# Performance work log

Hardware: AMD Instinct MI355X
Metric: run time of the kernel (lower is better)

Reference implementation:

```python
import jax, jax.numpy as jnp
import numpy as np

B, T, N, IN_DIM, H, C, L, S, P = 64, 13, 325, 2, 64, 4, 2, 4, 12
NC = S * N  # combined temporal-graph node count per batch element


def _make_adj(rng, n, density=0.03):
    mask = rng.random((n, n)) < density
    return (mask * rng.random((n, n))).astype(np.float32)


def _combine(adj, s, forward):
    n = adj.shape[0]
    out = np.zeros((n * s, n * s), np.float32)
    for i in range(s):
        out[i * n:(i + 1) * n, i * n:(i + 1) * n] = adj
        if forward and i < s - 1:
            out[i * n:(i + 1) * n, (i + 1) * n:(i + 2) * n] = np.eye(n, dtype=np.float32)
    return out


def _checkpoints(s, t):
    mark, cp = s, []
    while mark < t:
        cp.append(mark)
        mark += s - 1
    if cp[-1] != t:
        cp.append(t)
    return cp


def setup_inputs():
    key = jax.random.key(0)
    ks = jax.random.split(key, 20)
    rng = np.random.default_rng(0)
    adj = _make_adj(rng, N)
    pea = _make_adj(rng, N)
    sc = 0.05
    inp = {
        'inputs': jax.random.normal(ks[0], (B, T, N, IN_DIM), jnp.float32),
        'adj_fwd': jnp.asarray(_combine(adj, S, True)),
        'adj_bwd': jnp.asarray(_combine(adj, S, False)),
        'pea_fwd': jnp.asarray(_combine(pea, S, True)),
        'pea_bwd': jnp.asarray(_combine(pea, S, False)),
        'w_in': sc * jax.random.normal(ks[1], (IN_DIM, H), jnp.float32),
        'b_in': jnp.zeros((H,), jnp.float32),
        'res_w': sc * jax.random.normal(ks[2], (S,), jnp.float32),
        'res_b': jnp.zeros((), jnp.float32),
        'gconv_w': sc * jax.random.normal(ks[3], (S,), jnp.float32),
        'gconv_b': jnp.zeros((), jnp.float32),
        'gate1_w': sc * jax.random.normal(ks[4], (H, H), jnp.float32),
        'gate1_b': jnp.zeros((H,), jnp.float32),
        'gate2_w': sc * jax.random.normal(ks[5], (H, H * C), jnp.float32),
        'gate2_b': jnp.zeros((H * C,), jnp.float32),
        'reduce_w': sc * jax.random.normal(ks[6], (C * H, H), jnp.float32),
        'reduce_b': jnp.zeros((H,), jnp.float32),
        'gcn_adj_w': sc * jax.random.normal(ks[7], (C, L, 2, H, H), jnp.float32),
        'gcn_adj_b': jnp.zeros((C, L, H), jnp.float32),
        'gcn_pea_w': sc * jax.random.normal(ks[8], (C, L, 2, H, H), jnp.float32),
        'gcn_pea_b': jnp.zeros((C, L, H), jnp.float32),
        'out_conv_w': sc * jax.random.normal(ks[9], (P,), jnp.float32),
        'out_conv_b': jnp.zeros((P,), jnp.float32),
        'out_lin_w': sc * jax.random.normal(ks[10], (H, 1), jnp.float32),
        'out_lin_b': jnp.zeros((1,), jnp.float32),
    }
    return inp


def _gcn_stack(feats, W, b, A_f, A_b, n_out):
    # feats [B, S*N, H]; W [L, 2, H, H]; weighted message passing over both supports
    h = feats
    for l in range(W.shape[0]):
        mf = jnp.einsum('nm,bmh->bnh', A_f, h)
        mb = jnp.einsum('nm,bmh->bnh', A_b, h)
        h = jax.nn.relu(mf @ W[l, 0] + mb @ W[l, 1] + b[l])
    return h[:, -n_out:, :]  # last snapshot's nodes -> [B, N, H]


def reference(inputs, adj_fwd, adj_bwd, pea_fwd, pea_bwd, w_in, b_in, res_w, res_b,
              gconv_w, gconv_b, gate1_w, gate1_b, gate2_w, gate2_b, reduce_w, reduce_b,
              gcn_adj_w, gcn_adj_b, gcn_pea_w, gcn_pea_b, out_conv_w, out_conv_b,
              out_lin_w, out_lin_b):
    b_, t_, n_, _ = inputs.shape
    h_ = w_in.shape[1]
    s_ = res_w.shape[0]
    c_ = gcn_adj_w.shape[0]
    x = inputs @ w_in + b_in  # [B, T, N, H]
    last = None
    left = 0
    for idx, right in enumerate(_checkpoints(s_, t_)):
        fs = x[:, left:right] if idx == 0 else jnp.concatenate([last, x[:, left:right]], axis=1)  # [B,S,N,H]
        gf = (jnp.einsum('s,bsnh->bnh', gconv_w, fs) + gconv_b).reshape(b_ * n_, h_)
        residual = jnp.einsum('s,bsnh->bnh', res_w, fs) + res_b  # [B,N,H]
        feats = fs.reshape(b_, s_ * n_, h_)
        ca = jnp.concatenate(
            [_gcn_stack(feats, gcn_adj_w[c], gcn_adj_b[c], adj_fwd, adj_bwd, n_) for c in range(c_)],
            axis=-1).reshape(b_ * n_, c_ * h_)
        cp = jnp.concatenate(
            [_gcn_stack(feats, gcn_pea_w[c], gcn_pea_b[c], pea_fwd, pea_bwd, n_) for c in range(c_)],
            axis=-1).reshape(b_ * n_, c_ * h_)
        gate = jax.nn.sigmoid(jax.nn.relu(gf @ gate1_w + gate1_b) @ gate2_w + gate2_b)
        gr = gate * ca + (1.0 - gate) * cp
        gr = (gr @ reduce_w + reduce_b).reshape(b_, n_, h_)
        cr = gr + residual
        # nn.LayerNorm([B, N, H], elementwise_affine=False): normalize over whole tensor
        mu = jnp.mean(cr)
        var = jnp.var(cr)
        last = ((cr - mu) * jax.lax.rsqrt(var + 1e-5))[:, None]  # [B,1,N,H]
        left = right
    # 1x1 conv 1->pred_len over channel dim, then linear H->1
    out = jax.nn.relu(out_conv_w.reshape(1, -1, 1, 1) * last + out_conv_b.reshape(1, -1, 1, 1))
    out = out @ out_lin_w + out_lin_b  # [B, pred_len, N, 1]
    return out
```

## Files before the change

### kernel.cpp

```cpp
#include <hip/hip_runtime.h>
#include <hip/hip_bf16.h>
#include <math.h>

#define B_    64
#define T_    13
#define N_    325
#define H_    64
#define C_    4
#define L_    2
#define S_    4
#define P_    12
#define KCP   4
#define M_    (B_*N_)
#define ADJLD 1300
#define NNZCAP 64
#define WPITCH 72
#define MTP   264
#define RTP   264
#define NBLK  1300
#define MIXG  1304

typedef short bfrag __attribute__((ext_vector_type(8)));
typedef float f32x4 __attribute__((ext_vector_type(4)));

__device__ __forceinline__ void fma4(float4& a, float s, float4 x) {
    a.x += s * x.x; a.y += s * x.y; a.z += s * x.z; a.w += s * x.w;
}
__device__ __forceinline__ ushort bf_rne(float f) {
    unsigned u = __float_as_uint(f);
    return (ushort)((u + 0x7fffu + ((u >> 16) & 1u)) >> 16);
}
__device__ __forceinline__ uint2 pack_bf4(float4 v) {
    unsigned a = __float_as_uint(v.x), b = __float_as_uint(v.y);
    unsigned c = __float_as_uint(v.z), d = __float_as_uint(v.w);
    a = (a + 0x7fffu + ((a >> 16) & 1u)) >> 16;
    b = (b + 0x7fffu + ((b >> 16) & 1u)) >> 16;
    c = (c + 0x7fffu + ((c >> 16) & 1u)) >> 16;
    d = (d + 0x7fffu + ((d >> 16) & 1u)) >> 16;
    return make_uint2(a | (b << 16), c | (d << 16));
}
__device__ __forceinline__ float4 unpack_bf4(uint2 p) {
    return make_float4(__uint_as_float(p.x << 16),
                       __uint_as_float(p.x & 0xffff0000u),
                       __uint_as_float(p.y << 16),
                       __uint_as_float(p.y & 0xffff0000u));
}

__global__ void k_setup(
    const float* __restrict__ adj_fwd, const float* __restrict__ pea_fwd,
    const float* __restrict__ inp,
    const float* __restrict__ w_in, const float* __restrict__ b_in,
    const float* __restrict__ gadj_w, const float* __restrict__ gpea_w,
    const float* __restrict__ reduce_w,
    const float* __restrict__ gate1_w, const float* __restrict__ gate2_w,
    int* __restrict__ cnt, int* __restrict__ cols, float* __restrict__ vals,
    ushort* __restrict__ g_init4, ushort* __restrict__ WT,
    ushort* __restrict__ RT, ushort* __restrict__ W1T, ushort* __restrict__ W2T)
{
    int bid = blockIdx.x, t = threadIdx.x;
    if (bid >= 182) {
        int idx = (bid - 182) * 256 + t;
        if (idx >= 4 * M_ * H_) return;
        int h  = idx & 63;
        int r  = idx >> 6;
        int it = r / M_;
        int m  = r - it * M_;
        int b  = m / N_, n = m % N_;
        int tt = 3 * it + 3;
        const float* ip = inp + ((size_t)(b * T_ + tt) * N_ + n) * 2;
        g_init4[idx] = bf_rne(ip[0] * w_in[h] + ip[1] * w_in[H_ + h] + b_in[h]);
    } else if (bid < 163) {
        int lane = t & 63, w = t >> 6;
        int row = bid * 4 + w;
        if (row >= 2 * N_) return;
        int mat = (row >= N_) ? 1 : 0;
        int n   = row - mat * N_;
        const float* A = mat ? pea_fwd : adj_fwd;
        const float* rp = A + (size_t)n * ADJLD;
        int* cw   = cols + (size_t)row * NNZCAP;
        float* vw = vals + (size_t)row * NNZCAP;
        int c = 0;
        for (int c0 = 0; c0 < 384; c0 += 64) {
            int col = c0 + lane;
            float v = (col < N_) ? rp[col] : 0.f;
            unsigned long long mmask = __ballot(v != 0.f);
            int idx = c + __popcll(mmask & ((1ull << lane) - 1ull));
            if (v != 0.f && idx < NNZCAP) { cw[idx] = col; vw[idx] = v; }
            c += __popcll(mmask);
        }
        if (c + lane < NNZCAP) { cw[c + lane] = 0; vw[c + lane] = 0.f; }
        if (lane == 0) cnt[row] = (c < NNZCAP) ? c : NNZCAP;
    } else if (bid == 163) {
        for (int i = 0; i < 64; ++i) {
            int e = t + i * 256;
            int k = e >> 6, n = e & 63;
            RT[(size_t)n * RTP + k] = bf_rne(reduce_w[e]);
        }
    } else if (bid < 180) {
        int mat = bid - 164;
        int layer = mat >> 3, sm = mat & 7;
        int stack = sm >> 2, c = sm & 3;
        const float* w0 = (stack ? gpea_w : gadj_w) + (size_t)((c * L_ + layer) * 2) * 4096;
        const float* w1 = w0 + 4096;
        for (int i = 0; i < 16; ++i) {
            int e = t + i * 256;
            int k = e >> 6, n = e & 63;
            WT[((size_t)mat * 64 + n) * WPITCH + k] = bf_rne(w0[e] + w1[e]);
        }
    } else if (bid == 180) {
        for (int i = 0; i < 16; ++i) {
            int e = t + i * 256;
            int k = e >> 6, n = e & 63;
            W1T[(size_t)n * WPITCH + k] = bf_rne(gate1_w[e]);
        }
    } else {
        for (int i = 0; i < 64; ++i) {
            int e = t + i * 256;
            int k = e >> 8, n = e & 255;
            W2T[(size_t)n * WPITCH + k] = bf_rne(gate2_w[e]);
        }
    }
}

__device__ __forceinline__ void l1_block(
    int vb, int t,
    const int*   __restrict__ cnt,
    const int*   __restrict__ cols,
    const float* __restrict__ vals,
    const ushort* __restrict__ g_init,
    const ushort* __restrict__ WT,
    const float* __restrict__ badj, const float* __restrict__ bpea,
    ushort* __restrict__ G1a, ushort* __restrict__ G1p,
    ushort* MaH, ushort* MpH)
{
    int lane = t & 63, w = t >> 6;
    int m0 = vb * 32;
    int q = lane >> 4, ml = lane & 15;
    int colg = w * 16 + ml;

    bfrag BF[8][2];
    #pragma unroll
    for (int mat = 0; mat < 8; ++mat)
        #pragma unroll
        for (int kc = 0; kc < 2; ++kc)
            BF[mat][kc] = *(const bfrag*)&WT[((size_t)mat * 64 + colg) * WPITCH + kc * 32 + q * 8];

    {
        int cl = lane & 15, rr = lane >> 4;
        int mA = m0 + w * 8 + rr;
        int mB = mA + 4;
        int nA = mA % N_, nB = mB % N_;
        const ushort* gA = g_init + (size_t)(mA - nA) * H_ + cl * 4;
        const ushort* gB = g_init + (size_t)(mB - nB) * H_ + cl * 4;
        const int   *cA0 = cols + nA * NNZCAP,        *cB0 = cols + nB * NNZCAP;
        const float *vA0 = vals + nA * NNZCAP,        *vB0 = vals + nB * NNZCAP;
        const int   *cA1 = cols + (N_ + nA) * NNZCAP, *cB1 = cols + (N_ + nB) * NNZCAP;
        const float *vA1 = vals + (N_ + nA) * NNZCAP, *vB1 = vals + (N_ + nB) * NNZCAP;
        int jm = max(max(cnt[nA], cnt[nB]), max(cnt[N_ + nA], cnt[N_ + nB]));
        float4 aA0 = make_float4(0.f,0.f,0.f,0.f), aB0 = make_float4(0.f,0.f,0.f,0.f);
        float4 aA1 = make_float4(0.f,0.f,0.f,0.f), aB1 = make_float4(0.f,0.f,0.f,0.f);
        for (int j = 0; j < jm; j += 2) {
            fma4(aA0, vA0[j],   unpack_bf4(*(const uint2*)&gA[cA0[j]   * H_]));
            fma4(aA0, vA0[j+1], unpack_bf4(*(const uint2*)&gA[cA0[j+1] * H_]));
            fma4(aB0, vB0[j],   unpack_bf4(*(const uint2*)&gB[cB0[j]   * H_]));
            fma4(aB0, vB0[j+1], unpack_bf4(*(const uint2*)&gB[cB0[j+1] * H_]));
            fma4(aA1, vA1[j],   unpack_bf4(*(const uint2*)&gA[cA1[j]   * H_]));
            fma4(aA1, vA1[j+1], unpack_bf4(*(const uint2*)&gA[cA1[j+1] * H_]));
            fma4(aB1, vB1[j],   unpack_bf4(*(const uint2*)&gB[cB1[j]   * H_]));
            fma4(aB1, vB1[j+1], unpack_bf4(*(const uint2*)&gB[cB1[j+1] * H_]));
        }
        *(uint2*)&MaH[(w * 8 + rr) * WPITCH + cl * 4]     = pack_bf4(aA0);
        *(uint2*)&MaH[(w * 8 + 4 + rr) * WPITCH + cl * 4] = pack_bf4(aB0);
        *(uint2*)&MpH[(w * 8 + rr) * WPITCH + cl * 4]     = pack_bf4(aA1);
        *(uint2*)&MpH[(w * 8 + 4 + rr) * WPITCH + cl * 4] = pack_bf4(aB1);
    }
    __syncthreads();

    #pragma unroll
    for (int sc = 0; sc < 8; ++sc) {
        int stack = sc >> 2, c = sc & 3;
        const ushort* Msrc = stack ? MpH : MaH;
        float bv = (stack ? bpea : badj)[c * L_ * H_ + colg];
        ushort* Gout = stack ? G1p : G1a;
        #pragma unroll
        for (int r = 0; r < 2; ++r) {
            bfrag A0 = *(const bfrag*)&Msrc[(16 * r + ml) * WPITCH + q * 8];
            bfrag A1 = *(const bfrag*)&Msrc[(16 * r + ml) * WPITCH + 32 + q * 8];
            f32x4 acc = {0.f, 0.f, 0.f, 0.f};
            acc = __builtin_amdgcn_mfma_f32_16x16x32_bf16(A0, BF[sc][0], acc, 0, 0, 0);
            acc = __builtin_amdgcn_mfma_f32_16x16x32_bf16(A1, BF[sc][1], acc, 0, 0, 0);
            #pragma unroll
            for (int j = 0; j < 4; ++j) {
                float v = acc[j] + bv;
                v = v > 0.f ? v : 0.f;
                Gout[(size_t)(m0 + 16 * r + q * 4 + j) * 256 + c * 64 + colg] = bf_rne(v);
            }
        }
    }
}

__global__ __launch_bounds__(256, 4) void k_layer1(
    const int*   __restrict__ cnt,
    const int*   __restrict__ cols,
    const float* __restrict__ vals,
    const ushort* __restrict__ g_init4,
    int it0,
    const ushort* __restrict__ WT,
    const float* __restrict__ badj, const float* __restrict__ bpea,
    ushort* __restrict__ G1a4, ushort* __restrict__ G1p4)
{
    __shared__ __align__(16) ushort MaH[32 * WPITCH];
    __shared__ __align__(16) ushort MpH[32 * WPITCH];
    int itk = blockIdx.x / 656;
    int lx  = blockIdx.x - itk * 656;
    int vb = (lx & 7) * 82 + (lx >> 3);
    if (vb >= 650) return;
    l1_block(vb, threadIdx.x, cnt, cols, vals,
             g_init4 + (size_t)(it0 + itk) * M_ * H_, WT, badj, bpea,
             G1a4 + (size_t)itk * M_ * 256, G1p4 + (size_t)itk * M_ * 256,
             MaH, MpH);
}

__global__ __launch_bounds__(256, 4) void k_mix(
    const float* __restrict__ inp,
    const float* __restrict__ w_in, const float* __restrict__ b_in,
    const float* __restrict__ gconv_w, const float* __restrict__ gconv_b,
    const float* __restrict__ res_w,   const float* __restrict__ res_b,
    const float* __restrict__ cr_in, int it,
    const ushort* __restrict__ W1T, const float* __restrict__ b1,
    const ushort* __restrict__ W2T, const float* __restrict__ b2,
    const int*   __restrict__ cnt,
    const int*   __restrict__ cols,
    const float* __restrict__ vals,
    const ushort* __restrict__ G1a, const ushort* __restrict__ G1p,
    const ushort* __restrict__ WT,
    const float* __restrict__ badj, const float* __restrict__ bpea,
    const ushort* __restrict__ RT,
    const float* __restrict__ reduce_b,
    float* __restrict__ cr,
    const float* __restrict__ partials_in,
    float* __restrict__ partials,
    const ushort* __restrict__ g_init_l1,
    ushort* __restrict__ G1a_wr, ushort* __restrict__ G1p_wr)
{
    __shared__ __align__(16) ushort MtA[16 * MTP];
    __shared__ __align__(16) ushort MtP[16 * MTP];
    __shared__ __align__(16) ushort Gf[16 * WPITCH];
    __shared__ __align__(16) ushort Gr[16 * WPITCH];
    __shared__ float RES[16 * 68];
    __shared__ float red[8];
    int t = threadIdx.x, lane = t & 63, w = t >> 6;

    if (blockIdx.x >= MIXG) {
        int lx = blockIdx.x - MIXG;
        int vb1 = (lx & 7) * 82 + (lx >> 3);
        if (vb1 >= 650) return;
        l1_block(vb1, t, cnt, cols, vals, g_init_l1, WT, badj, bpea,
                 G1a_wr, G1p_wr, (ushort*)MtA, (ushort*)MtP);
        return;
    }

    int vb = (blockIdx.x & 7) * 163 + (blockIdx.x >> 3);
    if (vb >= NBLK) return;
    int m0 = vb * 16;
    int q = lane >> 4, ml = lane & 15;
    int colg = w * 16 + ml;

    float mu = 0.f, rs = 0.f;
    if (it > 0) {
        float a = 0.f, b = 0.f;
        for (int i = t; i < NBLK; i += 256) { a += partials_in[i]; b += partials_in[NBLK + i]; }
        #pragma unroll
        for (int off = 32; off > 0; off >>= 1) {
            a += __shfl_xor(a, off);
            b += __shfl_xor(b, off);
        }
        if (lane == 0) { red[w] = a; red[4 + w] = b; }
        __syncthreads();
        a = red[0] + red[1] + red[2] + red[3];
        b = red[4] + red[5] + red[6] + red[7];
        const float inv = 1.f / (float)(M_ * H_);
        mu = a * inv;
        float var = b * inv - mu * mu;
        rs = rsqrtf(var + 1e-5f);
    }

    {
        float wa = w_in[lane], wb = w_in[H_ + lane], bi = b_in[lane];
        float gw0 = gconv_w[0], gw1 = gconv_w[1], gw2 = gconv_w[2], gw3 = gconv_w[3];
        float rw0 = res_w[0],   rw1 = res_w[1],   rw2 = res_w[2],   rw3 = res_w[3];
        float gb = gconv_b[0],  rb = res_b[0];
        int t1 = (it == 0) ? 1 : (3 * it + 1);
        for (int i = 0; i < 4; ++i) {
            int r = i * 4 + w;
            int m = m0 + r;
            int b = m / N_, n = m % N_;
            const float* ipb = inp + ((size_t)b * T_ * N_ + n) * 2;
            float v0;
            if (it > 0) v0 = (cr_in[(size_t)m * H_ + lane] - mu) * rs;
            else        v0 = ipb[0] * wa + ipb[1] * wb + bi;
            const float* ip1 = ipb + (size_t)t1 * N_ * 2;
            const float* ip2 = ip1 + (size_t)N_ * 2;
            const float* ip3 = ip2 + (size_t)N_ * 2;
            float v1 = ip1[0] * wa + ip1[1] * wb + bi;
            float v2 = ip2[0] * wa + ip2[1] * wb + bi;
            float v3 = ip3[0] * wa + ip3[1] * wb + bi;
            Gf[r * WPITCH + lane] = bf_rne(gb + gw0 * v0 + gw1 * v1 + gw2 * v2 + gw3 * v3);
            RES[r * 68 + lane]    = rb + rw0 * v0 + rw1 * v1 + rw2 * v2 + rw3 * v3;
        }
    }
    __syncthreads();

    {
        bfrag A0 = *(const bfrag*)&Gf[ml * WPITCH + q * 8];
        bfrag A1 = *(const bfrag*)&Gf[ml * WPITCH + 32 + q * 8];
        bfrag B0 = *(const bfrag*)&W1T[(size_t)colg * WPITCH + q * 8];
        bfrag B1 = *(const bfrag*)&W1T[(size_t)colg * WPITCH + 32 + q * 8];
        f32x4 acc = {0.f, 0.f, 0.f, 0.f};
        acc = __builtin_amdgcn_mfma_f32_16x16x32_bf16(A0, B0, acc, 0, 0, 0);
        acc = __builtin_amdgcn_mfma_f32_16x16x32_bf16(A1, B1, acc, 0, 0, 0);
        float bb = b1[colg];
        #pragma unroll
        for (int j = 0; j < 4; ++j) {
            float v = acc[j] + bb;
            v = v > 0.f ? v : 0.f;
            Gr[(q * 4 + j) * WPITCH + colg] = bf_rne(v);
        }
    }
    __syncthreads();

    f32x4 gsv[4];
    {
        bfrag A0 = *(const bfrag*)&Gr[ml * WPITCH + q * 8];
        bfrag A1 = *(const bfrag*)&Gr[ml * WPITCH + 32 + q * 8];
        #pragma unroll
        for (int c = 0; c < 4; ++c) {
            bfrag B0 = *(const bfrag*)&W2T[(size_t)(c * 64 + colg) * WPITCH + q * 8];
            bfrag B1 = *(const bfrag*)&W2T[(size_t)(c * 64 + colg) * WPITCH + 32 + q * 8];
            f32x4 acc = {0.f, 0.f, 0.f, 0.f};
            acc = __builtin_amdgcn_mfma_f32_16x16x32_bf16(A0, B0, acc, 0, 0, 0);
            acc = __builtin_amdgcn_mfma_f32_16x16x32_bf16(A1, B1, acc, 0, 0, 0);
            float bb = b2[c * 64 + colg];
            #pragma unroll
            for (int j = 0; j < 4; ++j)
                gsv[c][j] = 1.f / (1.f + expf(-(acc[j] + bb)));
        }
    }

    for (int pp = 0; pp < 4; pp += 2) {
        int ma = m0 + w * 4 + pp, mb = ma + 1;
        int na = ma % N_, nb = mb % N_;
        const ushort* ga = G1a + (size_t)(ma - na) * 256 + lane * 4;
        const ushort* gb = G1a + (size_t)(mb - nb) * 256 + lane * 4;
        const ushort* pa = G1p + (size_t)(ma - na) * 256 + lane * 4;
        const ushort* pb = G1p + (size_t)(mb - nb) * 256 + lane * 4;
        const int   *cA0 = cols + na * NNZCAP,        *cB0 = cols + nb * NNZCAP;
        const float *vA0 = vals + na * NNZCAP,        *vB0 = vals + nb * NNZCAP;
        const int   *cA1 = cols + (N_ + na) * NNZCAP, *cB1 = cols + (N_ + nb) * NNZCAP;
        const float *vA1 = vals + (N_ + na) * NNZCAP, *vB1 = vals + (N_ + nb) * NNZCAP;
        int jm = max(max(cnt[na], cnt[nb]), max(cnt[N_ + na], cnt[N_ + nb]));
        float4 a0 = make_float4(0.f,0.f,0.f,0.f), a1 = make_float4(0.f,0.f,0.f,0.f);
        float4 p0 = make_float4(0.f,0.f,0.f,0.f), p1 = make_float4(0.f,0.f,0.f,0.f);
        for (int j = 0; j < jm; j += 2) {
            fma4(a0, vA0[j],   unpack_bf4(*(const uint2*)&ga[cA0[j]   * 256]));
            fma4(a0, vA0[j+1], unpack_bf4(*(const uint2*)&ga[cA0[j+1] * 256]));
            fma4(a1, vB0[j],   unpack_bf4(*(const uint2*)&gb[cB0[j]   * 256]));
            fma4(a1, vB0[j+1], unpack_bf4(*(const uint2*)&gb[cB0[j+1] * 256]));
            fma4(p0, vA1[j],   unpack_bf4(*(const uint2*)&pa[cA1[j]   * 256]));
            fma4(p0, vA1[j+1], unpack_bf4(*(const uint2*)&pa[cA1[j+1] * 256]));
            fma4(p1, vB1[j],   unpack_bf4(*(const uint2*)&pb[cB1[j]   * 256]));
            fma4(p1, vB1[j+1], unpack_bf4(*(const uint2*)&pb[cB1[j+1] * 256]));
        }
        int row0 = w * 4 + pp;
        *(uint2*)&MtA[row0 * MTP + lane * 4]       = pack_bf4(a0);
        *(uint2*)&MtA[(row0 + 1) * MTP + lane * 4] = pack_bf4(a1);
        *(uint2*)&MtP[row0 * MTP + lane * 4]       = pack_bf4(p0);
        *(uint2*)&MtP[(row0 + 1) * MTP + lane * 4] = pack_bf4(p1);
    }
    __syncthreads();

    const ushort* WT1 = WT + (size_t)8 * 64 * WPITCH;
    f32x4 res[4];
    bfrag B0c = *(const bfrag*)&WT1[(size_t)colg * WPITCH + q * 8];
    bfrag B1c = *(const bfrag*)&WT1[(size_t)colg * WPITCH + 32 + q * 8];
    #pragma unroll
    for (int sc = 0; sc < 8; ++sc) {
        int stack = sc >> 2, c = sc & 3;
        bfrag B0n = B0c, B1n = B1c;
        if (sc < 7) {
            B0n = *(const bfrag*)&WT1[((size_t)(sc + 1) * 64 + colg) * WPITCH + q * 8];
            B1n = *(const bfrag*)&WT1[((size_t)(sc + 1) * 64 + colg) * WPITCH + 32 + q * 8];
        }
        const ushort* Msrc = stack ? MtP : MtA;
        float bv = (stack ? bpea : badj)[(c * L_ + 1) * H_ + colg];
        bfrag A0 = *(const bfrag*)&Msrc[ml * MTP + c * 64 + q * 8];
        bfrag A1 = *(const bfrag*)&Msrc[ml * MTP + c * 64 + 32 + q * 8];
        f32x4 acc = {0.f, 0.f, 0.f, 0.f};
        acc = __builtin_amdgcn_mfma_f32_16x16x32_bf16(A0, B0c, acc, 0, 0, 0);
        acc = __builtin_amdgcn_mfma_f32_16x16x32_bf16(A1, B1c, acc, 0, 0, 0);
        #pragma unroll
        for (int j = 0; j < 4; ++j) {
            float v = acc[j] + bv;
            v = v > 0.f ? v : 0.f;
            if (stack == 0) res[c][j] = gsv[c][j] * v;
            else            res[c][j] += (1.f - gsv[c][j]) * v;
        }
        B0c = B0n; B1c = B1n;
    }

    bfrag RF[8];
    #pragma unroll
    for (int kc = 0; kc < 8; ++kc)
        RF[kc] = *(const bfrag*)&RT[(size_t)colg * RTP + kc * 32 + q * 8];
    f32x4 rv;
    #pragma unroll
    for (int j = 0; j < 4; ++j)
        rv[j] = RES[(q * 4 + j) * 68 + colg];

    __syncthreads();
    #pragma unroll
    for (int c = 0; c < 4; ++c)
        #pragma unroll
        for (int j = 0; j < 4; ++j)
            MtA[(q * 4 + j) * MTP + c * 64 + colg] = bf_rne(res[c][j]);
    __syncthreads();

    f32x4 racc = {0.f, 0.f, 0.f, 0.f};
    #pragma unroll
    for (int kc = 0; kc < 8; ++kc) {
        bfrag A0 = *(const bfrag*)&MtA[ml * MTP + kc * 32 + q * 8];
        racc = __builtin_amdgcn_mfma_f32_16x16x32_bf16(A0, RF[kc], racc, 0, 0, 0);
    }

    float bi = reduce_b[colg];
    float s = 0.f, s2 = 0.f;
    #pragma unroll
    for (int j = 0; j < 4; ++j) {
        int m = m0 + q * 4 + j;
        float v = racc[j] + bi + rv[j];
        cr[(size_t)m * 64 + colg] = v;
        s += v; s2 += v * v;
    }
    #pragma unroll
    for (int off = 32; off > 0; off >>= 1) {
        s  += __shfl_xor(s, off);
        s2 += __shfl_xor(s2, off);
    }
    if (lane == 0) { red[w] = s; red[4 + w] = s2; }
    __syncthreads();
    if (t == 0) partials[vb]        = red[0] + red[1] + red[2] + red[3];
    if (t == 1) partials[NBLK + vb] = red[4] + red[5] + red[6] + red[7];
}

__global__ __launch_bounds__(64) void k_out(
    const float* __restrict__ cr, const float* __restrict__ partials,
    const float* __restrict__ ocw, const float* __restrict__ ocb,
    const float* __restrict__ olw, const float* __restrict__ olb,
    float* __restrict__ out) {
    int t = threadIdx.x;
    float a = 0.f, b2s = 0.f;
    for (int i = t; i < NBLK; i += 64) { a += partials[i]; b2s += partials[NBLK + i]; }
    #pragma unroll
    for (int off = 32; off > 0; off >>= 1) {
        a   += __shfl_xor(a, off);
        b2s += __shfl_xor(b2s, off);
    }
    const float inv = 1.f / (float)(M_ * H_);
    float mu  = a * inv;
    float var = b2s * inv - mu * mu;
    float rs  = rsqrtf(var + 1e-5f);

    int m = blockIdx.x * 64 + t;
    int b = m / N_, n = m % N_;
    float cw[P_], cb[P_], acc[P_];
    #pragma unroll
    for (int p = 0; p < P_; ++p) { cw[p] = ocw[p]; cb[p] = ocb[p]; acc[p] = 0.f; }
    const float* lr = cr + (size_t)m * H_;
    for (int h4 = 0; h4 < 64; h4 += 4) {
        float4 lv4 = *(const float4*)&lr[h4];
        float4 wv4 = *(const float4*)&olw[h4];
        float lv[4] = {(lv4.x - mu) * rs, (lv4.y - mu) * rs,
                       (lv4.z - mu) * rs, (lv4.w - mu) * rs};
        float wv[4] = {wv4.x, wv4.y, wv4.z, wv4.w};
        #pragma unroll
        for (int e = 0; e < 4; ++e) {
            float lvv = lv[e], wvv = wv[e];
            #pragma unroll
            for (int p = 0; p < P_; ++p) {
                float u = cw[p] * lvv + cb[p];
                u = u > 0.f ? u : 0.f;
                acc[p] += u * wvv;
            }
        }
    }
    float ob = olb[0];
    #pragma unroll
    for (int p = 0; p < P_; ++p)
        out[(size_t)(b * P_ + p) * N_ + n] = acc[p] + ob;
}

extern "C" void kernel_launch(void* const* d_in, const int* in_sizes, int n_in,
                              void* d_out, int out_size, void* d_ws, size_t ws_size,
                              hipStream_t stream) {
    const float* inp      = (const float*)d_in[0];
    const float* adj_fwd  = (const float*)d_in[1];
    const float* pea_fwd  = (const float*)d_in[3];
    const float* w_in     = (const float*)d_in[5];
    const float* b_in     = (const float*)d_in[6];
    const float* res_w    = (const float*)d_in[7];
    const float* res_b    = (const float*)d_in[8];
    const float* gconv_w  = (const float*)d_in[9];
    const float* gconv_b  = (const float*)d_in[10];
    const float* gate1_w  = (const float*)d_in[11];
    const float* gate1_b  = (const float*)d_in[12];
    const float* gate2_w  = (const float*)d_in[13];
    const float* gate2_b  = (const float*)d_in[14];
    const float* reduce_w = (const float*)d_in[15];
    const float* reduce_b = (const float*)d_in[16];
    const float* gadj_w   = (const float*)d_in[17];
    const float* gadj_b   = (const float*)d_in[18];
    const float* gpea_w   = (const float*)d_in[19];
    const float* gpea_b   = (const float*)d_in[20];
    const float* ocw      = (const float*)d_in[21];
    const float* ocb      = (const float*)d_in[22];
    const float* olw      = (const float*)d_in[23];
    const float* olb      = (const float*)d_in[24];
    float* out = (float*)d_out;

    float* ws       = (float*)d_ws;
    float* cr       = ws;
    float* partials = cr + (size_t)M_ * H_;
    int*   scnt  = (int*)(partials + 2 * NBLK);
    int*   scols = scnt + 2 * N_;
    float* svals = (float*)(scols + 2 * N_ * NNZCAP);
    ushort* G1a4 = (ushort*)(svals + 2 * N_ * NNZCAP);
    ushort* G1p4 = G1a4 + 2 * (size_t)M_ * 256;
    ushort* g_init4 = G1p4 + 2 * (size_t)M_ * 256;
    ushort* WT   = g_init4 + 4 * (size_t)M_ * H_;
    WT = (ushort*)(((uintptr_t)WT + 15) & ~(uintptr_t)15);
    ushort* RT   = WT + 16 * 64 * WPITCH;
    ushort* W1T  = RT + 64 * RTP;
    ushort* W2T  = W1T + 64 * WPITCH;

    k_setup<<<182 + (4 * M_ * H_) / 256, 256, 0, stream>>>(
        adj_fwd, pea_fwd, inp, w_in, b_in, gadj_w, gpea_w, reduce_w,
        gate1_w, gate2_w, scnt, scols, svals, g_init4, WT, RT, W1T, W2T);

    k_layer1<<<1312, 256, 0, stream>>>(
        scnt, scols, svals, g_init4, 0, WT, gadj_b, gpea_b, G1a4, G1p4);

    for (int it = 0; it < 4; ++it) {
        int slot = it & 1;
        int embed = (it == 1 || it == 2);
        int grid  = MIXG + (embed ? 656 : 0);
        int wrsl  = (it + 1) & 1;
        k_mix<<<grid, 256, 0, stream>>>(
            inp, w_in, b_in, gconv_w, gconv_b, res_w, res_b, cr, it,
            W1T, gate1_b, W2T, gate2_b,
            scnt, scols, svals,
            G1a4 + (size_t)slot * M_ * 256, G1p4 + (size_t)slot * M_ * 256,
            WT, gadj_b, gpea_b, RT, reduce_b, cr, partials, partials,
            g_init4 + (size_t)(it + 1) * M_ * H_,
            G1a4 + (size_t)wrsl * M_ * 256, G1p4 + (size_t)wrsl * M_ * 256);
    }

    k_out<<<N_, 64, 0, stream>>>(cr, partials, ocw, ocb, olw, olb, out);
}
```

Before: 449.7 us.

## Halve k_mix row tile, embed first layer-1 in mix, stream layer weights

k_mix now processes 8 rows per block instead of 16, doubling the grid to 2600 blocks and raising launch bounds to 6 blocks per CU. The intent is to expose more parallelism and occupancy, at the cost of half-empty 16x16 MFMA tiles and more per-block overhead. The first layer-1 precompute now runs alone in k_layer1, and the next iteration's layer-1 is embedded into the it=0 mix launch as well. l1_block now double-buffers the weight fragments per matrix instead of holding all 16 in registers, to cut register pressure.

```diff
diff --git a/kernel.cpp b/kernel.cpp
--- a/kernel.cpp
+++ b/kernel.cpp
@@ -17,8 +17,8 @@
 #define WPITCH 72
 #define MTP   264
 #define RTP   264
-#define NBLK  1300
-#define MIXG  1304
+#define NBLK  2600
+#define MIXG  2600
 
 typedef short bfrag __attribute__((ext_vector_type(8)));
 typedef float f32x4 __attribute__((ext_vector_type(4)));
@@ -138,13 +138,6 @@
     int q = lane >> 4, ml = lane & 15;
     int colg = w * 16 + ml;
 
-    bfrag BF[8][2];
-    #pragma unroll
-    for (int mat = 0; mat < 8; ++mat)
-        #pragma unroll
-        for (int kc = 0; kc < 2; ++kc)
-            BF[mat][kc] = *(const bfrag*)&WT[((size_t)mat * 64 + colg) * WPITCH + kc * 32 + q * 8];
-
     {
         int cl = lane & 15, rr = lane >> 4;
         int mA = m0 + w * 8 + rr;
@@ -176,9 +169,16 @@
     }
     __syncthreads();
 
+    bfrag B0c = *(const bfrag*)&WT[(size_t)colg * WPITCH + q * 8];
+    bfrag B1c = *(const bfrag*)&WT[(size_t)colg * WPITCH + 32 + q * 8];
     #pragma unroll
     for (int sc = 0; sc < 8; ++sc) {
         int stack = sc >> 2, c = sc & 3;
+        bfrag B0n = B0c, B1n = B1c;
+        if (sc < 7) {
+            B0n = *(const bfrag*)&WT[((size_t)(sc + 1) * 64 + colg) * WPITCH + q * 8];
+            B1n = *(const bfrag*)&WT[((size_t)(sc + 1) * 64 + colg) * WPITCH + 32 + q * 8];
+        }
         const ushort* Msrc = stack ? MpH : MaH;
         float bv = (stack ? bpea : badj)[c * L_ * H_ + colg];
         ushort* Gout = stack ? G1p : G1a;
@@ -187,8 +187,8 @@
             bfrag A0 = *(const bfrag*)&Msrc[(16 * r + ml) * WPITCH + q * 8];
             bfrag A1 = *(const bfrag*)&Msrc[(16 * r + ml) * WPITCH + 32 + q * 8];
             f32x4 acc = {0.f, 0.f, 0.f, 0.f};
-            acc = __builtin_amdgcn_mfma_f32_16x16x32_bf16(A0, BF[sc][0], acc, 0, 0, 0);
-            acc = __builtin_amdgcn_mfma_f32_16x16x32_bf16(A1, BF[sc][1], acc, 0, 0, 0);
+            acc = __builtin_amdgcn_mfma_f32_16x16x32_bf16(A0, B0c, acc, 0, 0, 0);
+            acc = __builtin_amdgcn_mfma_f32_16x16x32_bf16(A1, B1c, acc, 0, 0, 0);
             #pragma unroll
             for (int j = 0; j < 4; ++j) {
                 float v = acc[j] + bv;
@@ -196,6 +196,7 @@
                 Gout[(size_t)(m0 + 16 * r + q * 4 + j) * 256 + c * 64 + colg] = bf_rne(v);
             }
         }
+        B0c = B0n; B1c = B1n;
     }
 }
 
@@ -204,24 +205,19 @@
     const int*   __restrict__ cols,
     const float* __restrict__ vals,
     const ushort* __restrict__ g_init4,
-    int it0,
     const ushort* __restrict__ WT,
     const float* __restrict__ badj, const float* __restrict__ bpea,
     ushort* __restrict__ G1a4, ushort* __restrict__ G1p4)
 {
     __shared__ __align__(16) ushort MaH[32 * WPITCH];
     __shared__ __align__(16) ushort MpH[32 * WPITCH];
-    int itk = blockIdx.x / 656;
-    int lx  = blockIdx.x - itk * 656;
-    int vb = (lx & 7) * 82 + (lx >> 3);
+    int vb = (blockIdx.x & 7) * 82 + (blockIdx.x >> 3);
     if (vb >= 650) return;
-    l1_block(vb, threadIdx.x, cnt, cols, vals,
-             g_init4 + (size_t)(it0 + itk) * M_ * H_, WT, badj, bpea,
-             G1a4 + (size_t)itk * M_ * 256, G1p4 + (size_t)itk * M_ * 256,
-             MaH, MpH);
-}
-
-__global__ __launch_bounds__(256, 4) void k_mix(
+    l1_block(vb, threadIdx.x, cnt, cols, vals, g_init4, WT, badj, bpea,
+             G1a4, G1p4, MaH, MpH);
+}
+
+__global__ __launch_bounds__(256, 6) void k_mix(
     const float* __restrict__ inp,
     const float* __restrict__ w_in, const float* __restrict__ b_in,
     const float* __restrict__ gconv_w, const float* __restrict__ gconv_b,
@@ -247,7 +243,7 @@
     __shared__ __align__(16) ushort MtP[16 * MTP];
     __shared__ __align__(16) ushort Gf[16 * WPITCH];
     __shared__ __align__(16) ushort Gr[16 * WPITCH];
-    __shared__ float RES[16 * 68];
+    __shared__ float RES[8 * 68];
     __shared__ float red[8];
     int t = threadIdx.x, lane = t & 63, w = t >> 6;
 
@@ -260,9 +256,8 @@
         return;
     }
 
-    int vb = (blockIdx.x & 7) * 163 + (blockIdx.x >> 3);
-    if (vb >= NBLK) return;
-    int m0 = vb * 16;
+    int vb = (blockIdx.x & 7) * 325 + (blockIdx.x >> 3);
+    int m0 = vb * 8;
     int q = lane >> 4, ml = lane & 15;
     int colg = w * 16 + ml;
 
@@ -291,7 +286,7 @@
         float rw0 = res_w[0],   rw1 = res_w[1],   rw2 = res_w[2],   rw3 = res_w[3];
         float gb = gconv_b[0],  rb = res_b[0];
         int t1 = (it == 0) ? 1 : (3 * it + 1);
-        for (int i = 0; i < 4; ++i) {
+        for (int i = 0; i < 2; ++i) {
             int r = i * 4 + w;
             int m = m0 + r;
             int b = m / N_, n = m % N_;
@@ -347,8 +342,8 @@
         }
     }
 
-    for (int pp = 0; pp < 4; pp += 2) {
-        int ma = m0 + w * 4 + pp, mb = ma + 1;
+    {
+        int ma = m0 + w * 2, mb = ma + 1;
         int na = ma % N_, nb = mb % N_;
         const ushort* ga = G1a + (size_t)(ma - na) * 256 + lane * 4;
         const ushort* gb = G1a + (size_t)(mb - nb) * 256 + lane * 4;
@@ -371,7 +366,7 @@
             fma4(p1, vB1[j],   unpack_bf4(*(const uint2*)&pb[cB1[j]   * 256]));
             fma4(p1, vB1[j+1], unpack_bf4(*(const uint2*)&pb[cB1[j+1] * 256]));
         }
-        int row0 = w * 4 + pp;
+        int row0 = w * 2;
         *(uint2*)&MtA[row0 * MTP + lane * 4]       = pack_bf4(a0);
         *(uint2*)&MtA[(row0 + 1) * MTP + lane * 4] = pack_bf4(a1);
         *(uint2*)&MtP[row0 * MTP + lane * 4]       = pack_bf4(p0);
@@ -415,7 +410,7 @@
     f32x4 rv;
     #pragma unroll
     for (int j = 0; j < 4; ++j)
-        rv[j] = RES[(q * 4 + j) * 68 + colg];
+        rv[j] = RES[(((q * 4 + j) & 7)) * 68 + colg];
 
     __syncthreads();
     #pragma unroll
@@ -434,12 +429,14 @@
 
     float bi = reduce_b[colg];
     float s = 0.f, s2 = 0.f;
-    #pragma unroll
-    for (int j = 0; j < 4; ++j) {
-        int m = m0 + q * 4 + j;
-        float v = racc[j] + bi + rv[j];
-        cr[(size_t)m * 64 + colg] = v;
-        s += v; s2 += v * v;
+    if (q < 2) {
+        #pragma unroll
+        for (int j = 0; j < 4; ++j) {
+            int m = m0 + q * 4 + j;
+            float v = racc[j] + bi + rv[j];
+            cr[(size_t)m * 64 + colg] = v;
+            s += v; s2 += v * v;
+        }
     }
     #pragma unroll
     for (int off = 32; off > 0; off >>= 1) {
@@ -546,12 +543,12 @@
         adj_fwd, pea_fwd, inp, w_in, b_in, gadj_w, gpea_w, reduce_w,
         gate1_w, gate2_w, scnt, scols, svals, g_init4, WT, RT, W1T, W2T);
 
-    k_layer1<<<1312, 256, 0, stream>>>(
-        scnt, scols, svals, g_init4, 0, WT, gadj_b, gpea_b, G1a4, G1p4);
+    k_layer1<<<656, 256, 0, stream>>>(
+        scnt, scols, svals, g_init4, WT, gadj_b, gpea_b, G1a4, G1p4);
 
     for (int it = 0; it < 4; ++it) {
         int slot = it & 1;
-        int embed = (it == 1 || it == 2);
+        int embed = (it < 3);
         int grid  = MIXG + (embed ? 656 : 0);
         int wrsl  = (it + 1) & 1;
         k_mix<<<grid, 256, 0, stream>>>(
@@ -560,7 +557,7 @@
             scnt, scols, svals,
             G1a4 + (size_t)slot * M_ * 256, G1p4 + (size_t)slot * M_ * 256,
             WT, gadj_b, gpea_b, RT, reduce_b, cr, partials, partials,
-            g_init4 + (size_t)(it + 1) * M_ * H_,
+            g_init4 + (size_t)((it + 1) & 3) * M_ * H_,
             G1a4 + (size_t)wrsl * M_ * 256, G1p4 + (size_t)wrsl * M_ * 256);
     }
 
```

Result: slower. 516.3 us (+14.8%).

## Fold input embedding through sparse adjacency instead of precomputing embedded features

Applied to the files above, without the earlier changes.

The rank-2 input embedding is linear, so the sparse adjacency aggregation is now applied directly to the 2-channel raw inputs. Each row accumulates sum v*x0, v*x1 and sum v, and the embedding weights and bias are applied afterwards. This removes the setup pass that wrote four 64-wide bf16 embedded feature tensors and cuts the gather traffic in the layer-1 aggregation from 64 bf16 values per neighbor to one float2. Rounding behavior changes slightly because the embedding is no longer quantized to bf16 before aggregation.

```diff
diff --git a/kernel.cpp b/kernel.cpp
--- a/kernel.cpp
+++ b/kernel.cpp
@@ -48,28 +48,15 @@
 
 __global__ void k_setup(
     const float* __restrict__ adj_fwd, const float* __restrict__ pea_fwd,
-    const float* __restrict__ inp,
-    const float* __restrict__ w_in, const float* __restrict__ b_in,
     const float* __restrict__ gadj_w, const float* __restrict__ gpea_w,
     const float* __restrict__ reduce_w,
     const float* __restrict__ gate1_w, const float* __restrict__ gate2_w,
     int* __restrict__ cnt, int* __restrict__ cols, float* __restrict__ vals,
-    ushort* __restrict__ g_init4, ushort* __restrict__ WT,
+    ushort* __restrict__ WT,
     ushort* __restrict__ RT, ushort* __restrict__ W1T, ushort* __restrict__ W2T)
 {
     int bid = blockIdx.x, t = threadIdx.x;
-    if (bid >= 182) {
-        int idx = (bid - 182) * 256 + t;
-        if (idx >= 4 * M_ * H_) return;
-        int h  = idx & 63;
-        int r  = idx >> 6;
-        int it = r / M_;
-        int m  = r - it * M_;
-        int b  = m / N_, n = m % N_;
-        int tt = 3 * it + 3;
-        const float* ip = inp + ((size_t)(b * T_ + tt) * N_ + n) * 2;
-        g_init4[idx] = bf_rne(ip[0] * w_in[h] + ip[1] * w_in[H_ + h] + b_in[h]);
-    } else if (bid < 163) {
+    if (bid < 163) {
         int lane = t & 63, w = t >> 6;
         int row = bid * 4 + w;
         if (row >= 2 * N_) return;
@@ -123,11 +110,12 @@
 }
 
 __device__ __forceinline__ void l1_block(
-    int vb, int t,
+    int vb, int t, int tt,
     const int*   __restrict__ cnt,
     const int*   __restrict__ cols,
     const float* __restrict__ vals,
-    const ushort* __restrict__ g_init,
+    const float* __restrict__ inp,
+    const float* __restrict__ w_in, const float* __restrict__ b_in,
     const ushort* __restrict__ WT,
     const float* __restrict__ badj, const float* __restrict__ bpea,
     ushort* __restrict__ G1a, ushort* __restrict__ G1p,
@@ -146,33 +134,34 @@
             BF[mat][kc] = *(const bfrag*)&WT[((size_t)mat * 64 + colg) * WPITCH + kc * 32 + q * 8];
 
     {
-        int cl = lane & 15, rr = lane >> 4;
-        int mA = m0 + w * 8 + rr;
-        int mB = mA + 4;
-        int nA = mA % N_, nB = mB % N_;
-        const ushort* gA = g_init + (size_t)(mA - nA) * H_ + cl * 4;
-        const ushort* gB = g_init + (size_t)(mB - nB) * H_ + cl * 4;
-        const int   *cA0 = cols + nA * NNZCAP,        *cB0 = cols + nB * NNZCAP;
-        const float *vA0 = vals + nA * NNZCAP,        *vB0 = vals + nB * NNZCAP;
-        const int   *cA1 = cols + (N_ + nA) * NNZCAP, *cB1 = cols + (N_ + nB) * NNZCAP;
-        const float *vA1 = vals + (N_ + nA) * NNZCAP, *vB1 = vals + (N_ + nB) * NNZCAP;
-        int jm = max(max(cnt[nA], cnt[nB]), max(cnt[N_ + nA], cnt[N_ + nB]));
-        float4 aA0 = make_float4(0.f,0.f,0.f,0.f), aB0 = make_float4(0.f,0.f,0.f,0.f);
-        float4 aA1 = make_float4(0.f,0.f,0.f,0.f), aB1 = make_float4(0.f,0.f,0.f,0.f);
-        for (int j = 0; j < jm; j += 2) {
-            fma4(aA0, vA0[j],   unpack_bf4(*(const uint2*)&gA[cA0[j]   * H_]));
-            fma4(aA0, vA0[j+1], unpack_bf4(*(const uint2*)&gA[cA0[j+1] * H_]));
-            fma4(aB0, vB0[j],   unpack_bf4(*(const uint2*)&gB[cB0[j]   * H_]));
-            fma4(aB0, vB0[j+1], unpack_bf4(*(const uint2*)&gB[cB0[j+1] * H_]));
-            fma4(aA1, vA1[j],   unpack_bf4(*(const uint2*)&gA[cA1[j]   * H_]));
-            fma4(aA1, vA1[j+1], unpack_bf4(*(const uint2*)&gA[cA1[j+1] * H_]));
-            fma4(aB1, vB1[j],   unpack_bf4(*(const uint2*)&gB[cB1[j]   * H_]));
-            fma4(aB1, vB1[j+1], unpack_bf4(*(const uint2*)&gB[cB1[j+1] * H_]));
-        }
-        *(uint2*)&MaH[(w * 8 + rr) * WPITCH + cl * 4]     = pack_bf4(aA0);
-        *(uint2*)&MaH[(w * 8 + 4 + rr) * WPITCH + cl * 4] = pack_bf4(aB0);
-        *(uint2*)&MpH[(w * 8 + rr) * WPITCH + cl * 4]     = pack_bf4(aA1);
-        *(uint2*)&MpH[(w * 8 + 4 + rr) * WPITCH + cl * 4] = pack_bf4(aB1);
+        int row_l  = lane & 7;
+        int stackl = (lane >> 3) & 1;
+        int part   = lane >> 4;
+        int m = m0 + w * 8 + row_l;
+        int b = m / N_;
+        int n = m - b * N_;
+        const float* ipb = inp + ((size_t)(b * T_ + tt) * N_) * 2;
+        int rowidx = stackl * N_ + n;
+        const int*   cp = cols + (size_t)rowidx * NNZCAP;
+        const float* vp = vals + (size_t)rowidx * NNZCAP;
+        int myc = cnt[rowidx];
+        float s0 = 0.f, s1 = 0.f, sv = 0.f;
+        for (int j = part; j < myc; j += 4) {
+            int c   = cp[j];
+            float v = vp[j];
+            float2 x = *(const float2*)&ipb[(size_t)c * 2];
+            s0 += v * x.x; s1 += v * x.y; sv += v;
+        }
+        s0 += __shfl_xor(s0, 16); s1 += __shfl_xor(s1, 16); sv += __shfl_xor(sv, 16);
+        s0 += __shfl_xor(s0, 32); s1 += __shfl_xor(s1, 32); sv += __shfl_xor(sv, 32);
+        float wa = w_in[lane], wb = w_in[H_ + lane], bi = b_in[lane];
+        #pragma unroll
+        for (int r = 0; r < 8; ++r) {
+            float a0 = __shfl(s0, r),     a1 = __shfl(s1, r),     av = __shfl(sv, r);
+            float p0 = __shfl(s0, 8 + r), p1 = __shfl(s1, 8 + r), pv = __shfl(sv, 8 + r);
+            MaH[(w * 8 + r) * WPITCH + lane] = bf_rne(a0 * wa + a1 * wb + av * bi);
+            MpH[(w * 8 + r) * WPITCH + lane] = bf_rne(p0 * wa + p1 * wb + pv * bi);
+        }
     }
     __syncthreads();
 
@@ -203,7 +192,8 @@
     const int*   __restrict__ cnt,
     const int*   __restrict__ cols,
     const float* __restrict__ vals,
-    const ushort* __restrict__ g_init4,
+    const float* __restrict__ inp,
+    const float* __restrict__ w_in, const float* __restrict__ b_in,
     int it0,
     const ushort* __restrict__ WT,
     const float* __restrict__ badj, const float* __restrict__ bpea,
@@ -215,8 +205,8 @@
     int lx  = blockIdx.x - itk * 656;
     int vb = (lx & 7) * 82 + (lx >> 3);
     if (vb >= 650) return;
-    l1_block(vb, threadIdx.x, cnt, cols, vals,
-             g_init4 + (size_t)(it0 + itk) * M_ * H_, WT, badj, bpea,
+    l1_block(vb, threadIdx.x, 3 * (it0 + itk) + 3, cnt, cols, vals,
+             inp, w_in, b_in, WT, badj, bpea,
              G1a4 + (size_t)itk * M_ * 256, G1p4 + (size_t)itk * M_ * 256,
              MaH, MpH);
 }
@@ -240,7 +230,7 @@
     float* __restrict__ cr,
     const float* __restrict__ partials_in,
     float* __restrict__ partials,
-    const ushort* __restrict__ g_init_l1,
+    int tt_l1,
     ushort* __restrict__ G1a_wr, ushort* __restrict__ G1p_wr)
 {
     __shared__ __align__(16) ushort MtA[16 * MTP];
@@ -255,8 +245,8 @@
         int lx = blockIdx.x - MIXG;
         int vb1 = (lx & 7) * 82 + (lx >> 3);
         if (vb1 >= 650) return;
-        l1_block(vb1, t, cnt, cols, vals, g_init_l1, WT, badj, bpea,
-                 G1a_wr, G1p_wr, (ushort*)MtA, (ushort*)MtP);
+        l1_block(vb1, t, tt_l1, cnt, cols, vals, inp, w_in, b_in,
+                 WT, badj, bpea, G1a_wr, G1p_wr, (ushort*)MtA, (ushort*)MtP);
         return;
     }
 
@@ -535,19 +525,18 @@
     float* svals = (float*)(scols + 2 * N_ * NNZCAP);
     ushort* G1a4 = (ushort*)(svals + 2 * N_ * NNZCAP);
     ushort* G1p4 = G1a4 + 2 * (size_t)M_ * 256;
-    ushort* g_init4 = G1p4 + 2 * (size_t)M_ * 256;
-    ushort* WT   = g_init4 + 4 * (size_t)M_ * H_;
+    ushort* WT   = G1p4 + 2 * (size_t)M_ * 256;
     WT = (ushort*)(((uintptr_t)WT + 15) & ~(uintptr_t)15);
     ushort* RT   = WT + 16 * 64 * WPITCH;
     ushort* W1T  = RT + 64 * RTP;
     ushort* W2T  = W1T + 64 * WPITCH;
 
-    k_setup<<<182 + (4 * M_ * H_) / 256, 256, 0, stream>>>(
-        adj_fwd, pea_fwd, inp, w_in, b_in, gadj_w, gpea_w, reduce_w,
-        gate1_w, gate2_w, scnt, scols, svals, g_init4, WT, RT, W1T, W2T);
+    k_setup<<<182, 256, 0, stream>>>(
+        adj_fwd, pea_fwd, gadj_w, gpea_w, reduce_w,
+        gate1_w, gate2_w, scnt, scols, svals, WT, RT, W1T, W2T);
 
     k_layer1<<<1312, 256, 0, stream>>>(
-        scnt, scols, svals, g_init4, 0, WT, gadj_b, gpea_b, G1a4, G1p4);
+        scnt, scols, svals, inp, w_in, b_in, 0, WT, gadj_b, gpea_b, G1a4, G1p4);
 
     for (int it = 0; it < 4; ++it) {
         int slot = it & 1;
@@ -560,7 +549,7 @@
             scnt, scols, svals,
             G1a4 + (size_t)slot * M_ * 256, G1p4 + (size_t)slot * M_ * 256,
             WT, gadj_b, gpea_b, RT, reduce_b, cr, partials, partials,
-            g_init4 + (size_t)(it + 1) * M_ * H_,
+            3 * (it + 1) + 3,
             G1a4 + (size_t)wrsl * M_ * 256, G1p4 + (size_t)wrsl * M_ * 256);
     }
 
```

Result: faster. 403.9 us (-10.2%).
